# Performance work log

Measured on AMD Instinct MI355X. Metric: run time of the kernel, lower is better.

## Reference

```python
import jax, jax.numpy as jnp
import numpy as np

N_NODES = 50000
N_EDGES = 800000
HID = 256
MAX_ID = 10000

def _gcn(x, w, b, src, dst, ew, n):
    # PyG GCNConv with self-loops (weight 1.0): out = D^-1/2 (A+I) D^-1/2 (x W) + b
    xw = x @ w                                                   # [N, out]
    deg = jax.ops.segment_sum(ew, dst, num_segments=n) + 1.0     # self-loop adds 1
    dinv = jax.lax.rsqrt(deg)                                    # [N]
    norm = dinv[src] * ew * dinv[dst]                            # [E]
    agg = jax.ops.segment_sum(norm[:, None] * xw[src], dst, num_segments=n)
    agg = agg + (dinv * dinv)[:, None] * xw                      # self-loop term
    return agg + b

def setup_inputs() -> dict:
    key = jax.random.key(0)
    ks = jax.random.split(key, 24)
    s = 0.05
    inp = {
        "node_features": jax.random.normal(ks[0], (N_NODES, 3), jnp.float32),
        "edge_index": jax.random.randint(ks[1], (2, N_EDGES), 0, N_NODES),
        "edge_ids": jax.random.randint(ks[2], (N_EDGES,), 0, MAX_ID + 1),
        "edge_pos": jax.random.randint(ks[3], (N_EDGES,), 0, 3),
        "id_embed": jax.random.normal(ks[4], (MAX_ID + 1, 8), jnp.float32) * s,
        "pos_embed": jax.random.normal(ks[5], (3, 2), jnp.float32) * s,
        "ew_w1": jax.random.normal(ks[6], (10, 10), jnp.float32) * s,
        "ew_b1": jnp.zeros((10,), jnp.float32),
        "ew_w2": jax.random.normal(ks[7], (10, 1), jnp.float32) * s,
        "ew_b2": jnp.zeros((1,), jnp.float32),
        "conv1_w": jax.random.normal(ks[8], (3, HID), jnp.float32) * s,
        "conv1_b": jnp.zeros((HID,), jnp.float32),
        "conv2_w": jax.random.normal(ks[9], (HID, HID), jnp.float32) * s,
        "conv2_b": jnp.zeros((HID,), jnp.float32),
        "actor_w1": jax.random.normal(ks[10], (2 * HID, HID), jnp.float32) * s,
        "actor_b1": jnp.zeros((HID,), jnp.float32),
        "actor_w2": jax.random.normal(ks[11], (HID, 1), jnp.float32) * s,
        "actor_b2": jnp.zeros((1,), jnp.float32),
        "critic_w1": jax.random.normal(ks[12], (2 * HID, 2 * HID), jnp.float32) * s,
        "critic_b1": jnp.zeros((2 * HID,), jnp.float32),
        "critic_w2": jax.random.normal(ks[13], (2 * HID, HID), jnp.float32) * s,
        "critic_b2": jnp.zeros((HID,), jnp.float32),
        "critic_w3": jax.random.normal(ks[14], (HID, 1), jnp.float32) * s,
        "critic_b3": jnp.zeros((1,), jnp.float32),
    }
    return inp

def reference(node_features, edge_index, edge_ids, edge_pos, id_embed, pos_embed,
              ew_w1, ew_b1, ew_w2, ew_b2, conv1_w, conv1_b, conv2_w, conv2_b,
              actor_w1, actor_b1, actor_w2, actor_b2,
              critic_w1, critic_b1, critic_w2, critic_b2, critic_w3, critic_b3):
    n = node_features.shape[0]
    src, dst = edge_index[0], edge_index[1]
    # edge weight MLP: Linear-ReLU-Linear-Sigmoid on [id_embed(8) | pos_embed(2)]
    feat = jnp.concatenate([id_embed[edge_ids], pos_embed[edge_pos]], axis=1)  # [E,10]
    h = jax.nn.relu(feat @ ew_w1 + ew_b1)
    ew = jax.nn.sigmoid(h @ ew_w2 + ew_b2)[:, 0]                               # [E]
    # two GCN layers with ReLU
    x = jax.nn.relu(_gcn(node_features, conv1_w, conv1_b, src, dst, ew, n))
    x = jax.nn.relu(_gcn(x, conv2_w, conv2_b, src, dst, ew, n))
    # global mean pooling + concat
    g = jnp.mean(x, axis=0)                                                    # [H]
    combined = jnp.concatenate([x, jnp.broadcast_to(g, (n, g.shape[0]))], axis=1)
    # actor head
    a = jax.nn.relu(combined @ actor_w1 + actor_b1)
    action_logits = (a @ actor_w2 + actor_b2)[:, 0]                            # [N]
    # critic head on pooled features
    pooled = jnp.mean(combined, axis=0)[None, :]                               # [1,2H]
    c = jax.nn.relu(pooled @ critic_w1 + critic_b1)
    c = jax.nn.relu(c @ critic_w2 + critic_b2)
    state_value = (c @ critic_w3 + critic_b3)[0, 0]                            # scalar
    return action_logits, state_value
```

## Files before the change

### kernel.cpp

```cpp
#include <hip/hip_runtime.h>
#include <math.h>

#define HID 256

typedef __attribute__((ext_vector_type(8))) short short8;
typedef __attribute__((ext_vector_type(4))) float floatx4;

__device__ __forceinline__ ushort bf16_rne(float x) {
    uint u = __float_as_uint(x);
    uint r = (u + 0x7FFFu + ((u >> 16) & 1u)) >> 16;
    return (ushort)r;
}
__device__ __forceinline__ float bf16_to_f(ushort h) {
    return __uint_as_float(((uint)h) << 16);
}

__global__ void k_edge(const int* __restrict__ eid, const int* __restrict__ epos,
                       const float* __restrict__ id_emb, const float* __restrict__ pos_emb,
                       const float* __restrict__ w1, const float* __restrict__ b1,
                       const float* __restrict__ w2, const float* __restrict__ b2,
                       const int* __restrict__ ei, float* __restrict__ ew,
                       unsigned long long* __restrict__ cnt64, int E) {
    __shared__ float sW1[100];
    __shared__ float sB1[10];
    __shared__ float sW2[10];
    __shared__ float sB2;
    int t = threadIdx.x;
    if (t < 100) sW1[t] = w1[t];
    if (t < 10) { sB1[t] = b1[t]; sW2[t] = w2[t]; }
    if (t == 0) sB2 = b2[0];
    __syncthreads();
    int e = blockIdx.x * blockDim.x + t;
    if (e >= E) return;
    int id = eid[e];
    int p  = epos[e];
    const float4* ide = (const float4*)(id_emb + (size_t)id * 8);
    float4 fa = ide[0], fb = ide[1];
    float f[10];
    f[0] = fa.x; f[1] = fa.y; f[2] = fa.z; f[3] = fa.w;
    f[4] = fb.x; f[5] = fb.y; f[6] = fb.z; f[7] = fb.w;
    f[8] = pos_emb[p * 2 + 0];
    f[9] = pos_emb[p * 2 + 1];
    float acc = sB2;
#pragma unroll
    for (int j = 0; j < 10; j++) {
        float h = sB1[j];
#pragma unroll
        for (int i = 0; i < 10; i++) h += f[i] * sW1[i * 10 + j];
        h = fmaxf(h, 0.f);
        acc += h * sW2[j];
    }
    float w = 1.f / (1.f + expf(-acc));
    ew[e] = w;
    int dst = ei[E + e];
    unsigned long long pack = (1ull << 40) + (unsigned long long)(w * 1048576.0f + 0.5f);
    atomicAdd(&cnt64[dst], pack);
}

__global__ void k_scan_a(const unsigned long long* __restrict__ cnt64,
                         int* __restrict__ row_ptr, int* __restrict__ bsums,
                         float* __restrict__ deg, const float* __restrict__ nf,
                         float4* __restrict__ nf4, float* __restrict__ gsum,
                         const float* __restrict__ w2, const float* __restrict__ aw1,
                         ushort* __restrict__ w2h, ushort* __restrict__ w2l,
                         ushort* __restrict__ a1h, ushort* __restrict__ a1l, int N) {
    __shared__ int s[256];
    int b = blockIdx.x, t = threadIdx.x;
    int i = b * 256 + t;
    if (b == 0) gsum[t] = 0.f;
    if (b < 64) {
        int gid = b * 256 + t;
        int mat = gid >> 13;
        int rem = gid & 8191;
        int c = rem >> 10;
        int tt = (rem >> 6) & 15;
        int L = rem & 63;
        int k0 = 32 * c + (L >> 4) * 8;
        int n  = 16 * tt + (L & 15);
        const float* W = mat ? aw1 : w2;
        ushort* H  = mat ? a1h : w2h;
        ushort* Lo = mat ? a1l : w2l;
        short8 hv, lv;
#pragma unroll
        for (int j = 0; j < 8; j++) {
            float x = W[(size_t)(k0 + j) * HID + n];
            ushort h = bf16_rne(x);
            hv[j] = (short)h;
            lv[j] = (short)bf16_rne(x - bf16_to_f(h));
        }
        size_t off = (size_t)rem * 8;
        *(short8*)(H + off) = hv;
        *(short8*)(Lo + off) = lv;
    }
    int v = 0;
    if (i < N) {
        unsigned long long cv = cnt64[i];
        v = (int)(cv >> 40);
        float degf = (float)(cv & 0xFFFFFFFFFFull) * (1.0f / 1048576.0f);
        deg[i] = 1.f / sqrtf(degf + 1.f);
        nf4[i] = make_float4(nf[i * 3 + 0], nf[i * 3 + 1], nf[i * 3 + 2], 0.f);
    }
    s[t] = v;
    __syncthreads();
    for (int off = 1; off < 256; off <<= 1) {
        int u = (t >= off) ? s[t - off] : 0;
        __syncthreads();
        s[t] += u;
        __syncthreads();
    }
    int incl = s[t];
    if (i < N) row_ptr[i] = incl - v;
    if (t == 255) bsums[b] = incl;
}

__global__ void k_scan_c(int* __restrict__ row_ptr, int* __restrict__ cursor,
                         const int* __restrict__ bsums, int N, int NB) {
    __shared__ int s[256];
    int b = blockIdx.x, t = threadIdx.x;
    int v = (t < NB) ? bsums[t] : 0;
    s[t] = (t < b) ? v : 0;
    __syncthreads();
    for (int off = 128; off > 0; off >>= 1) {
        if (t < off) s[t] += s[t + off];
        __syncthreads();
    }
    int boff = s[0];
    int i = b * 256 + t;
    if (i < N) {
        int rp = row_ptr[i] + boff;
        row_ptr[i] = rp;
        cursor[i] = rp;
    }
    if (b == NB - 1) {
        __syncthreads();
        s[t] = (t < NB) ? bsums[t] : 0;
        __syncthreads();
        for (int off = 128; off > 0; off >>= 1) {
            if (t < off) s[t] += s[t + off];
            __syncthreads();
        }
        if (t == 0) row_ptr[N] = s[0];
    }
}

__global__ void k_fill(const int* __restrict__ ei, const float* __restrict__ ew,
                       const float* __restrict__ dinv, int* __restrict__ cursor,
                       int2* __restrict__ csr, int E) {
    int e = blockIdx.x * blockDim.x + threadIdx.x;
    if (e >= E) return;
    int src = ei[e];
    int dst = ei[E + e];
    int slot = atomicAdd(&cursor[dst], 1);
    float norm = dinv[src] * ew[e] * dinv[dst];
    csr[slot] = make_int2(src, __float_as_int(norm));
}

__global__ void k_agg3(const int* __restrict__ row_ptr, const int2* __restrict__ csr,
                       const float4* __restrict__ nf4, const float* __restrict__ dinv,
                       float4* __restrict__ T3, int N) {
    int n = blockIdx.x * blockDim.x + threadIdx.x;
    if (n >= N) return;
    int s = row_ptr[n];
    int e = row_ptr[n + 1];
    float ax = 0.f, ay = 0.f, az = 0.f;
    int i = s;
    for (; i + 4 <= e; i += 4) {
        int2 c0 = csr[i], c1 = csr[i + 1], c2 = csr[i + 2], c3 = csr[i + 3];
        float4 t0 = nf4[c0.x], t1 = nf4[c1.x], t2 = nf4[c2.x], t3 = nf4[c3.x];
        float w0 = __int_as_float(c0.y), w1 = __int_as_float(c1.y);
        float w2 = __int_as_float(c2.y), w3 = __int_as_float(c3.y);
        ax = fmaf(w0, t0.x, ax); ay = fmaf(w0, t0.y, ay); az = fmaf(w0, t0.z, az);
        ax = fmaf(w1, t1.x, ax); ay = fmaf(w1, t1.y, ay); az = fmaf(w1, t1.z, az);
        ax = fmaf(w2, t2.x, ax); ay = fmaf(w2, t2.y, ay); az = fmaf(w2, t2.z, az);
        ax = fmaf(w3, t3.x, ax); ay = fmaf(w3, t3.y, ay); az = fmaf(w3, t3.z, az);
    }
    for (; i < e; i++) {
        int2 sn = csr[i];
        float w = __int_as_float(sn.y);
        float4 v = nf4[sn.x];
        ax = fmaf(w, v.x, ax);
        ay = fmaf(w, v.y, ay);
        az = fmaf(w, v.z, az);
    }
    float d = dinv[n];
    float dd = d * d;
    float4 v = nf4[n];
    ax = fmaf(dd, v.x, ax);
    ay = fmaf(dd, v.y, ay);
    az = fmaf(dd, v.z, az);
    T3[n] = make_float4(ax, ay, az, 0.f);
}

__device__ __forceinline__ void gf_edge(float4 t, float wgt,
                                        const float4& w0, const float4& w1,
                                        const float4& w2, const float4& bv, float4& acc) {
    float xx = fmaxf(fmaf(t.x, w0.x, fmaf(t.y, w1.x, fmaf(t.z, w2.x, bv.x))), 0.f);
    float xy = fmaxf(fmaf(t.x, w0.y, fmaf(t.y, w1.y, fmaf(t.z, w2.y, bv.y))), 0.f);
    float xz = fmaxf(fmaf(t.x, w0.z, fmaf(t.y, w1.z, fmaf(t.z, w2.z, bv.z))), 0.f);
    float xw = fmaxf(fmaf(t.x, w0.w, fmaf(t.y, w1.w, fmaf(t.z, w2.w, bv.w))), 0.f);
    acc.x = fmaf(wgt, xx, acc.x);
    acc.y = fmaf(wgt, xy, acc.y);
    acc.z = fmaf(wgt, xz, acc.z);
    acc.w = fmaf(wgt, xw, acc.w);
}

__global__ void k_gatherfused(const int* __restrict__ row_ptr, const int2* __restrict__ csr,
                              const float4* __restrict__ T3, const float* __restrict__ dinv,
                              const float* __restrict__ cw, const float* __restrict__ cb,
                              ushort* __restrict__ Ah, ushort* __restrict__ Al, int N) {
    int lane = threadIdx.x & 63;
    int wv = threadIdx.x >> 6;
    int n = blockIdx.x * 4 + wv;
    if (n >= N) return;
    const float4 w0 = *(const float4*)(cw + 4 * lane);
    const float4 w1 = *(const float4*)(cw + HID + 4 * lane);
    const float4 w2 = *(const float4*)(cw + 2 * HID + 4 * lane);
    const float4 bv = *(const float4*)(cb + 4 * lane);
    int s = row_ptr[n];
    int e = row_ptr[n + 1];
    float4 acc = make_float4(0.f, 0.f, 0.f, 0.f);
    int i = s;
    for (; i + 4 <= e; i += 4) {
        int2 c0 = csr[i], c1 = csr[i + 1], c2 = csr[i + 2], c3 = csr[i + 3];
        float4 t0 = T3[c0.x], t1 = T3[c1.x], t2 = T3[c2.x], t3 = T3[c3.x];
        gf_edge(t0, __int_as_float(c0.y), w0, w1, w2, bv, acc);
        gf_edge(t1, __int_as_float(c1.y), w0, w1, w2, bv, acc);
        gf_edge(t2, __int_as_float(c2.y), w0, w1, w2, bv, acc);
        gf_edge(t3, __int_as_float(c3.y), w0, w1, w2, bv, acc);
    }
    for (; i < e; i++) {
        int2 sn = csr[i];
        gf_edge(T3[sn.x], __int_as_float(sn.y), w0, w1, w2, bv, acc);
    }
    float d = dinv[n];
    gf_edge(T3[n], d * d, w0, w1, w2, bv, acc);
    ushort4 hv, lv;
    ushort h;
    h = bf16_rne(acc.x); hv.x = h; lv.x = bf16_rne(acc.x - bf16_to_f(h));
    h = bf16_rne(acc.y); hv.y = h; lv.y = bf16_rne(acc.y - bf16_to_f(h));
    h = bf16_rne(acc.z); hv.z = h; lv.z = bf16_rne(acc.z - bf16_to_f(h));
    h = bf16_rne(acc.w); hv.w = h; lv.w = bf16_rne(acc.w - bf16_to_f(h));
    size_t base = (size_t)n * HID + lane * 4;
    *(ushort4*)(Ah + base) = hv;
    *(ushort4*)(Al + base) = lv;
}

#define ASTRIDE 264

__global__ __launch_bounds__(256, 2) void k_gemm_mfma(
        const ushort* __restrict__ Ah, const ushort* __restrict__ Al,
        const float* __restrict__ b2,
        const ushort* __restrict__ w2h, const ushort* __restrict__ w2l,
        const ushort* __restrict__ a1h, const ushort* __restrict__ a1l,
        float* __restrict__ P, float* __restrict__ gsum, int N) {
    __shared__ ushort Hs[64 * ASTRIDE];
    __shared__ ushort Ls[64 * ASTRIDE];
    int tid = threadIdx.x;
    int n0 = blockIdx.x * 64;
    int w = tid >> 6;
    int L = tid & 63;
    int quad = L >> 4, ln = L & 15;

    int arow[4];
#pragma unroll
    for (int mt = 0; mt < 4; mt++) {
        int r = n0 + mt * 16 + ln;
        arow[mt] = (r < N) ? r : (N - 1);
    }

    floatx4 acc[4][4];
#pragma unroll
    for (int i = 0; i < 4; i++)
#pragma unroll
        for (int j = 0; j < 4; j++) acc[i][j] = 0.f;
    {
        short8 pah[2][4], pal[2][4], pbh[2][4], pbl[2][4];
#pragma unroll
        for (int mt = 0; mt < 4; mt++) {
            size_t ab = (size_t)arow[mt] * HID + quad * 8;
            pah[0][mt] = *(const short8*)(Ah + ab);
            pal[0][mt] = *(const short8*)(Al + ab);
        }
#pragma unroll
        for (int nt = 0; nt < 4; nt++) {
            size_t off = ((size_t)(4 * w + nt) * 64 + L) * 8;
            pbh[0][nt] = *(const short8*)(w2h + off);
            pbl[0][nt] = *(const short8*)(w2l + off);
        }
#pragma unroll
        for (int c = 0; c < 8; c++) {
            int cur = c & 1, nxt = cur ^ 1;
            if (c < 7) {
#pragma unroll
                for (int mt = 0; mt < 4; mt++) {
                    size_t ab = (size_t)arow[mt] * HID + 32 * (c + 1) + quad * 8;
                    pah[nxt][mt] = *(const short8*)(Ah + ab);
                    pal[nxt][mt] = *(const short8*)(Al + ab);
                }
#pragma unroll
                for (int nt = 0; nt < 4; nt++) {
                    size_t off = ((size_t)((c + 1) * 16 + 4 * w + nt) * 64 + L) * 8;
                    pbh[nxt][nt] = *(const short8*)(w2h + off);
                    pbl[nxt][nt] = *(const short8*)(w2l + off);
                }
            }
#pragma unroll
            for (int nt = 0; nt < 4; nt++) {
#pragma unroll
                for (int mt = 0; mt < 4; mt++) {
                    acc[nt][mt] = __builtin_amdgcn_mfma_f32_16x16x32_bf16(pah[cur][mt], pbh[cur][nt], acc[nt][mt], 0, 0, 0);
                    acc[nt][mt] = __builtin_amdgcn_mfma_f32_16x16x32_bf16(pah[cur][mt], pbl[cur][nt], acc[nt][mt], 0, 0, 0);
                    acc[nt][mt] = __builtin_amdgcn_mfma_f32_16x16x32_bf16(pal[cur][mt], pbh[cur][nt], acc[nt][mt], 0, 0, 0);
                }
            }
        }
    }

#pragma unroll
    for (int nt = 0; nt < 4; nt++) {
        int col = (4 * w + nt) * 16 + ln;
        float bb = b2[col];
        float s = 0.f;
#pragma unroll
        for (int mt = 0; mt < 4; mt++) {
#pragma unroll
            for (int r = 0; r < 4; r++) {
                int row = n0 + mt * 16 + quad * 4 + r;
                float v = fmaxf(acc[nt][mt][r] + bb, 0.f);
                acc[nt][mt][r] = v;
                if (row < N) s += v;
            }
        }
        s += __shfl_down(s, 32, 64);
        s += __shfl_down(s, 16, 64);
        if (L < 16) atomicAdd(&gsum[col], s);
    }

#pragma unroll
    for (int nt = 0; nt < 4; nt++) {
        int col = (4 * w + nt) * 16 + ln;
#pragma unroll
        for (int mt = 0; mt < 4; mt++) {
#pragma unroll
            for (int r = 0; r < 4; r++) {
                int row = mt * 16 + quad * 4 + r;
                float v = acc[nt][mt][r];
                ushort h = bf16_rne(v);
                Hs[row * ASTRIDE + col] = h;
                Ls[row * ASTRIDE + col] = bf16_rne(v - bf16_to_f(h));
            }
        }
    }
    __syncthreads();

    floatx4 acc2[4][4];
#pragma unroll
    for (int i = 0; i < 4; i++)
#pragma unroll
        for (int j = 0; j < 4; j++) acc2[i][j] = 0.f;
    {
        short8 pbh[2][4], pbl[2][4];
#pragma unroll
        for (int nt = 0; nt < 4; nt++) {
            size_t off = ((size_t)(4 * w + nt) * 64 + L) * 8;
            pbh[0][nt] = *(const short8*)(a1h + off);
            pbl[0][nt] = *(const short8*)(a1l + off);
        }
#pragma unroll
        for (int c = 0; c < 8; c++) {
            int cur = c & 1, nxt = cur ^ 1;
            if (c < 7) {
#pragma unroll
                for (int nt = 0; nt < 4; nt++) {
                    size_t off = ((size_t)((c + 1) * 16 + 4 * w + nt) * 64 + L) * 8;
                    pbh[nxt][nt] = *(const short8*)(a1h + off);
                    pbl[nxt][nt] = *(const short8*)(a1l + off);
                }
            }
            short8 ahf[4], alf[4];
#pragma unroll
            for (int mt = 0; mt < 4; mt++) {
                int base = (mt * 16 + ln) * ASTRIDE + 32 * c + quad * 8;
                ahf[mt] = *(const short8*)&Hs[base];
                alf[mt] = *(const short8*)&Ls[base];
            }
#pragma unroll
            for (int nt = 0; nt < 4; nt++) {
#pragma unroll
                for (int mt = 0; mt < 4; mt++) {
                    acc2[nt][mt] = __builtin_amdgcn_mfma_f32_16x16x32_bf16(ahf[mt], pbh[cur][nt], acc2[nt][mt], 0, 0, 0);
                    acc2[nt][mt] = __builtin_amdgcn_mfma_f32_16x16x32_bf16(ahf[mt], pbl[cur][nt], acc2[nt][mt], 0, 0, 0);
                    acc2[nt][mt] = __builtin_amdgcn_mfma_f32_16x16x32_bf16(alf[mt], pbh[cur][nt], acc2[nt][mt], 0, 0, 0);
                }
            }
        }
    }

#pragma unroll
    for (int nt = 0; nt < 4; nt++) {
        int col = (4 * w + nt) * 16 + ln;
#pragma unroll
        for (int mt = 0; mt < 4; mt++) {
#pragma unroll
            for (int r = 0; r < 4; r++) {
                int row = n0 + mt * 16 + quad * 4 + r;
                if (row < N) P[(size_t)row * HID + col] = acc2[nt][mt][r];
            }
        }
    }
}

__global__ void k_headsA(const float* __restrict__ gsum,
                         const float* __restrict__ cw1, const float* __restrict__ cb1,
                         float* __restrict__ c1g,
                         const float* __restrict__ aw1, const float* __restrict__ ab1,
                         float* __restrict__ gbias,
                         const float* __restrict__ cb3, float* __restrict__ sv_out,
                         float invN) {
    __shared__ float part[4][64];
    int b = blockIdx.x, t = threadIdx.x;
    int c = t & 63;
    int kr = t >> 6;
    if (b == 0 && t == 0) sv_out[0] = cb3[0];
    if (b < 8) {
        int col = b * 64 + c;
        float s = 0.f;
        for (int k = kr * 128; k < kr * 128 + 128; k++)
            s += gsum[k & (HID - 1)] * invN * cw1[(size_t)k * 512 + col];
        part[kr][c] = s;
        __syncthreads();
        if (kr == 0) {
            float v = cb1[col] + part[0][c] + part[1][c] + part[2][c] + part[3][c];
            c1g[col] = fmaxf(v, 0.f);
        }
    } else {
        int col = (b - 8) * 64 + c;
        float s = 0.f;
        for (int k = kr * 64; k < kr * 64 + 64; k++)
            s += gsum[k] * invN * aw1[(size_t)(HID + k) * HID + col];
        part[kr][c] = s;
        __syncthreads();
        if (kr == 0)
            gbias[col] = ab1[col] + part[0][c] + part[1][c] + part[2][c] + part[3][c];
    }
}

__global__ void k_headsB(const float* __restrict__ c1g,
                         const float* __restrict__ cw2, const float* __restrict__ cb2,
                         const float* __restrict__ cw3, float* __restrict__ sv_out) {
    __shared__ float part[4][64];
    int b = blockIdx.x, t = threadIdx.x;
    int c = t & 63;
    int kr = t >> 6;
    int col = b * 64 + c;
    float s = 0.f;
    for (int k = kr * 128; k < kr * 128 + 128; k++)
        s += c1g[k] * cw2[(size_t)k * HID + col];
    part[kr][c] = s;
    __syncthreads();
    if (kr == 0) {
        float v = fmaxf(cb2[col] + part[0][c] + part[1][c] + part[2][c] + part[3][c], 0.f)
                * cw3[col];
#pragma unroll
        for (int off = 32; off > 0; off >>= 1) v += __shfl_down(v, off, 64);
        if (c == 0) atomicAdd(sv_out, v);
    }
}

__global__ void k_logits(const float* __restrict__ P, const float* __restrict__ gbias,
                         const float* __restrict__ aw2, const float* __restrict__ ab2,
                         float* __restrict__ out, int N) {
    int lane = threadIdx.x & 63;
    int wv = threadIdx.x >> 6;
    int n = blockIdx.x * 4 + wv;
    if (n >= N) return;
    float4 p = *(const float4*)(P + (size_t)n * HID + 4 * lane);
    float4 gb = *(const float4*)(gbias + 4 * lane);
    float4 w2 = *(const float4*)(aw2 + 4 * lane);
    float v = fmaxf(p.x + gb.x, 0.f) * w2.x
            + fmaxf(p.y + gb.y, 0.f) * w2.y
            + fmaxf(p.z + gb.z, 0.f) * w2.z
            + fmaxf(p.w + gb.w, 0.f) * w2.w;
#pragma unroll
    for (int off = 32; off > 0; off >>= 1) v += __shfl_down(v, off, 64);
    if (lane == 0) out[n] = v + ab2[0];
}

extern "C" void kernel_launch(void* const* d_in, const int* in_sizes, int n_in,
                              void* d_out, int out_size, void* d_ws, size_t ws_size,
                              hipStream_t stream) {
    const float* nf      = (const float*)d_in[0];
    const int*   ei      = (const int*)d_in[1];
    const int*   eid     = (const int*)d_in[2];
    const int*   epos    = (const int*)d_in[3];
    const float* id_emb  = (const float*)d_in[4];
    const float* pos_emb = (const float*)d_in[5];
    const float* ew_w1   = (const float*)d_in[6];
    const float* ew_b1   = (const float*)d_in[7];
    const float* ew_w2   = (const float*)d_in[8];
    const float* ew_b2   = (const float*)d_in[9];
    const float* c1w     = (const float*)d_in[10];
    const float* c1b     = (const float*)d_in[11];
    const float* c2w     = (const float*)d_in[12];
    const float* c2b     = (const float*)d_in[13];
    const float* aw1     = (const float*)d_in[14];
    const float* ab1     = (const float*)d_in[15];
    const float* aw2     = (const float*)d_in[16];
    const float* ab2     = (const float*)d_in[17];
    const float* cw1     = (const float*)d_in[18];
    const float* cb1     = (const float*)d_in[19];
    const float* cw2     = (const float*)d_in[20];
    const float* cb2     = (const float*)d_in[21];
    const float* cw3     = (const float*)d_in[22];
    const float* cb3     = (const float*)d_in[23];

    int N = in_sizes[0] / 3;
    int E = in_sizes[2];
    int NB = (N + 255) / 256;
    float invN = 1.f / (float)N;

    char* ws = (char*)d_ws;
    unsigned long long* cnt64 = (unsigned long long*)ws;  ws += (size_t)N * 8;
    float* gsum     = (float*)ws;                         ws += HID * 4;
    float* deg      = (float*)ws;                         ws += (size_t)N * 4;
    ushort* Ah      = (ushort*)ws;                        ws += (size_t)N * HID * 2;
    ushort* Al      = (ushort*)ws;                        ws += (size_t)N * HID * 2;
    float* P        = (float*)ws;                         ws += (size_t)N * HID * 4;
    float* ew       = (float*)ws;                         ws += (size_t)E * 4;
    int2*  csr      = (int2*)ws;                          ws += (size_t)E * 8;
    int*   row_ptr  = (int*)ws;                           ws += (size_t)(N + 1) * 4;
    int*   cursor   = (int*)ws;                           ws += (size_t)N * 4;
    int*   bsums    = (int*)ws;                           ws += 256 * 4;
    float4* T3      = (float4*)ws;                        ws += (size_t)N * 16;
    float4* nf4     = (float4*)ws;                        ws += (size_t)N * 16;
    float* gbias    = (float*)ws;                         ws += HID * 4;
    float* c1g      = (float*)ws;                         ws += 512 * 4;
    ushort* w2h     = (ushort*)ws;                        ws += 65536 * 2;
    ushort* w2l     = (ushort*)ws;                        ws += 65536 * 2;
    ushort* a1h     = (ushort*)ws;                        ws += 65536 * 2;
    ushort* a1l     = (ushort*)ws;                        ws += 65536 * 2;

    float* out = (float*)d_out;

    hipMemsetAsync(cnt64, 0, (size_t)N * 8, stream);

    k_edge<<<(E + 255) / 256, 256, 0, stream>>>(eid, epos, id_emb, pos_emb,
                                                ew_w1, ew_b1, ew_w2, ew_b2, ei, ew, cnt64, E);

    k_scan_a<<<NB, 256, 0, stream>>>(cnt64, row_ptr, bsums, deg, nf, nf4, gsum,
                                     c2w, aw1, w2h, w2l, a1h, a1l, N);
    k_scan_c<<<NB, 256, 0, stream>>>(row_ptr, cursor, bsums, N, NB);

    k_fill<<<(E + 255) / 256, 256, 0, stream>>>(ei, ew, deg, cursor, csr, E);

    k_agg3<<<(N + 255) / 256, 256, 0, stream>>>(row_ptr, csr, nf4, deg, T3, N);

    k_gatherfused<<<(N + 3) / 4, 256, 0, stream>>>(row_ptr, csr, T3, deg, c1w, c1b, Ah, Al, N);

    k_gemm_mfma<<<(N + 63) / 64, 256, 0, stream>>>(Ah, Al, c2b, w2h, w2l, a1h, a1l, P, gsum, N);

    k_headsA<<<12, 256, 0, stream>>>(gsum, cw1, cb1, c1g, aw1, ab1, gbias,
                                     cb3, out + N, invN);
    k_headsB<<<4, 256, 0, stream>>>(c1g, cw2, cb2, cw3, out + N);

    k_logits<<<(N + 3) / 4, 256, 0, stream>>>(P, gbias, aw2, ab2, out, N);
}
```

Baseline: 376.0 us.

## Shrink GEMM row tile, deepen gather unroll, merge head kernels, two edges per fill thread

The MFMA GEMM tile drops from 64 to 48 rows with launch bounds raised to 3 blocks per CU, trading per-block reuse for occupancy. Both gather loops now unroll by 8 with loads batched ahead of the math to put more memory requests in flight. The critic-head kernel and the logits kernel are merged into one launch, and k_fill handles two edges per thread. The aim is to cut launch overhead and raise memory-level parallelism, at the cost of more register pressure in the unrolled loops.

Measured after the change: 390.6 us. 3.9% more time.

```diff
diff --git a/kernel.cpp b/kernel.cpp
--- a/kernel.cpp
+++ b/kernel.cpp
@@ -145,14 +145,23 @@
 
 __global__ void k_fill(const int* __restrict__ ei, const float* __restrict__ ew,
                        const float* __restrict__ dinv, int* __restrict__ cursor,
-                       int2* __restrict__ csr, int E) {
-    int e = blockIdx.x * blockDim.x + threadIdx.x;
-    if (e >= E) return;
-    int src = ei[e];
-    int dst = ei[E + e];
-    int slot = atomicAdd(&cursor[dst], 1);
-    float norm = dinv[src] * ew[e] * dinv[dst];
-    csr[slot] = make_int2(src, __float_as_int(norm));
+                       int2* __restrict__ csr, int E, int Eh) {
+    int g = blockIdx.x * blockDim.x + threadIdx.x;
+    if (g < Eh) {
+        int src = ei[g];
+        int dst = ei[E + g];
+        float norm = dinv[src] * ew[g] * dinv[dst];
+        int slot = atomicAdd(&cursor[dst], 1);
+        csr[slot] = make_int2(src, __float_as_int(norm));
+    }
+    int e2 = g + Eh;
+    if (e2 < E) {
+        int src = ei[e2];
+        int dst = ei[E + e2];
+        float norm = dinv[src] * ew[e2] * dinv[dst];
+        int slot = atomicAdd(&cursor[dst], 1);
+        csr[slot] = make_int2(src, __float_as_int(norm));
+    }
 }
 
 __global__ void k_agg3(const int* __restrict__ row_ptr, const int2* __restrict__ csr,
@@ -164,15 +173,20 @@
     int e = row_ptr[n + 1];
     float ax = 0.f, ay = 0.f, az = 0.f;
     int i = s;
-    for (; i + 4 <= e; i += 4) {
-        int2 c0 = csr[i], c1 = csr[i + 1], c2 = csr[i + 2], c3 = csr[i + 3];
-        float4 t0 = nf4[c0.x], t1 = nf4[c1.x], t2 = nf4[c2.x], t3 = nf4[c3.x];
-        float w0 = __int_as_float(c0.y), w1 = __int_as_float(c1.y);
-        float w2 = __int_as_float(c2.y), w3 = __int_as_float(c3.y);
-        ax = fmaf(w0, t0.x, ax); ay = fmaf(w0, t0.y, ay); az = fmaf(w0, t0.z, az);
-        ax = fmaf(w1, t1.x, ax); ay = fmaf(w1, t1.y, ay); az = fmaf(w1, t1.z, az);
-        ax = fmaf(w2, t2.x, ax); ay = fmaf(w2, t2.y, ay); az = fmaf(w2, t2.z, az);
-        ax = fmaf(w3, t3.x, ax); ay = fmaf(w3, t3.y, ay); az = fmaf(w3, t3.z, az);
+    for (; i + 8 <= e; i += 8) {
+        int2 c[8];
+        float4 t[8];
+#pragma unroll
+        for (int j = 0; j < 8; j++) c[j] = csr[i + j];
+#pragma unroll
+        for (int j = 0; j < 8; j++) t[j] = nf4[c[j].x];
+#pragma unroll
+        for (int j = 0; j < 8; j++) {
+            float w = __int_as_float(c[j].y);
+            ax = fmaf(w, t[j].x, ax);
+            ay = fmaf(w, t[j].y, ay);
+            az = fmaf(w, t[j].z, az);
+        }
     }
     for (; i < e; i++) {
         int2 sn = csr[i];
@@ -220,13 +234,16 @@
     int e = row_ptr[n + 1];
     float4 acc = make_float4(0.f, 0.f, 0.f, 0.f);
     int i = s;
-    for (; i + 4 <= e; i += 4) {
-        int2 c0 = csr[i], c1 = csr[i + 1], c2 = csr[i + 2], c3 = csr[i + 3];
-        float4 t0 = T3[c0.x], t1 = T3[c1.x], t2 = T3[c2.x], t3 = T3[c3.x];
-        gf_edge(t0, __int_as_float(c0.y), w0, w1, w2, bv, acc);
-        gf_edge(t1, __int_as_float(c1.y), w0, w1, w2, bv, acc);
-        gf_edge(t2, __int_as_float(c2.y), w0, w1, w2, bv, acc);
-        gf_edge(t3, __int_as_float(c3.y), w0, w1, w2, bv, acc);
+    for (; i + 8 <= e; i += 8) {
+        int2 c[8];
+        float4 t[8];
+#pragma unroll
+        for (int j = 0; j < 8; j++) c[j] = csr[i + j];
+#pragma unroll
+        for (int j = 0; j < 8; j++) t[j] = T3[c[j].x];
+#pragma unroll
+        for (int j = 0; j < 8; j++)
+            gf_edge(t[j], __int_as_float(c[j].y), w0, w1, w2, bv, acc);
     }
     for (; i < e; i++) {
         int2 sn = csr[i];
@@ -246,37 +263,39 @@
 }
 
 #define ASTRIDE 264
-
-__global__ __launch_bounds__(256, 2) void k_gemm_mfma(
+#define MT 3
+#define TROWS 48
+
+__global__ __launch_bounds__(256, 3) void k_gemm_mfma(
         const ushort* __restrict__ Ah, const ushort* __restrict__ Al,
         const float* __restrict__ b2,
         const ushort* __restrict__ w2h, const ushort* __restrict__ w2l,
         const ushort* __restrict__ a1h, const ushort* __restrict__ a1l,
         float* __restrict__ P, float* __restrict__ gsum, int N) {
-    __shared__ ushort Hs[64 * ASTRIDE];
-    __shared__ ushort Ls[64 * ASTRIDE];
+    __shared__ ushort Hs[TROWS * ASTRIDE];
+    __shared__ ushort Ls[TROWS * ASTRIDE];
     int tid = threadIdx.x;
-    int n0 = blockIdx.x * 64;
+    int n0 = blockIdx.x * TROWS;
     int w = tid >> 6;
     int L = tid & 63;
     int quad = L >> 4, ln = L & 15;
 
-    int arow[4];
-#pragma unroll
-    for (int mt = 0; mt < 4; mt++) {
+    int arow[MT];
+#pragma unroll
+    for (int mt = 0; mt < MT; mt++) {
         int r = n0 + mt * 16 + ln;
         arow[mt] = (r < N) ? r : (N - 1);
     }
 
-    floatx4 acc[4][4];
+    floatx4 acc[4][MT];
 #pragma unroll
     for (int i = 0; i < 4; i++)
 #pragma unroll
-        for (int j = 0; j < 4; j++) acc[i][j] = 0.f;
+        for (int j = 0; j < MT; j++) acc[i][j] = 0.f;
     {
-        short8 pah[2][4], pal[2][4], pbh[2][4], pbl[2][4];
-#pragma unroll
-        for (int mt = 0; mt < 4; mt++) {
+        short8 pah[2][MT], pal[2][MT], pbh[2][4], pbl[2][4];
+#pragma unroll
+        for (int mt = 0; mt < MT; mt++) {
             size_t ab = (size_t)arow[mt] * HID + quad * 8;
             pah[0][mt] = *(const short8*)(Ah + ab);
             pal[0][mt] = *(const short8*)(Al + ab);
@@ -292,7 +311,7 @@
             int cur = c & 1, nxt = cur ^ 1;
             if (c < 7) {
 #pragma unroll
-                for (int mt = 0; mt < 4; mt++) {
+                for (int mt = 0; mt < MT; mt++) {
                     size_t ab = (size_t)arow[mt] * HID + 32 * (c + 1) + quad * 8;
                     pah[nxt][mt] = *(const short8*)(Ah + ab);
                     pal[nxt][mt] = *(const short8*)(Al + ab);
@@ -307,7 +326,7 @@
 #pragma unroll
             for (int nt = 0; nt < 4; nt++) {
 #pragma unroll
-                for (int mt = 0; mt < 4; mt++) {
+                for (int mt = 0; mt < MT; mt++) {
                     acc[nt][mt] = __builtin_amdgcn_mfma_f32_16x16x32_bf16(pah[cur][mt], pbh[cur][nt], acc[nt][mt], 0, 0, 0);
                     acc[nt][mt] = __builtin_amdgcn_mfma_f32_16x16x32_bf16(pah[cur][mt], pbl[cur][nt], acc[nt][mt], 0, 0, 0);
                     acc[nt][mt] = __builtin_amdgcn_mfma_f32_16x16x32_bf16(pal[cur][mt], pbh[cur][nt], acc[nt][mt], 0, 0, 0);
@@ -322,7 +341,7 @@
         float bb = b2[col];
         float s = 0.f;
 #pragma unroll
-        for (int mt = 0; mt < 4; mt++) {
+        for (int mt = 0; mt < MT; mt++) {
 #pragma unroll
             for (int r = 0; r < 4; r++) {
                 int row = n0 + mt * 16 + quad * 4 + r;
@@ -340,7 +359,7 @@
     for (int nt = 0; nt < 4; nt++) {
         int col = (4 * w + nt) * 16 + ln;
 #pragma unroll
-        for (int mt = 0; mt < 4; mt++) {
+        for (int mt = 0; mt < MT; mt++) {
 #pragma unroll
             for (int r = 0; r < 4; r++) {
                 int row = mt * 16 + quad * 4 + r;
@@ -353,11 +372,11 @@
     }
     __syncthreads();
 
-    floatx4 acc2[4][4];
+    floatx4 acc2[4][MT];
 #pragma unroll
     for (int i = 0; i < 4; i++)
 #pragma unroll
-        for (int j = 0; j < 4; j++) acc2[i][j] = 0.f;
+        for (int j = 0; j < MT; j++) acc2[i][j] = 0.f;
     {
         short8 pbh[2][4], pbl[2][4];
 #pragma unroll
@@ -377,9 +396,9 @@
                     pbl[nxt][nt] = *(const short8*)(a1l + off);
                 }
             }
-            short8 ahf[4], alf[4];
-#pragma unroll
-            for (int mt = 0; mt < 4; mt++) {
+            short8 ahf[MT], alf[MT];
+#pragma unroll
+            for (int mt = 0; mt < MT; mt++) {
                 int base = (mt * 16 + ln) * ASTRIDE + 32 * c + quad * 8;
                 ahf[mt] = *(const short8*)&Hs[base];
                 alf[mt] = *(const short8*)&Ls[base];
@@ -387,7 +406,7 @@
 #pragma unroll
             for (int nt = 0; nt < 4; nt++) {
 #pragma unroll
-                for (int mt = 0; mt < 4; mt++) {
+                for (int mt = 0; mt < MT; mt++) {
                     acc2[nt][mt] = __builtin_amdgcn_mfma_f32_16x16x32_bf16(ahf[mt], pbh[cur][nt], acc2[nt][mt], 0, 0, 0);
                     acc2[nt][mt] = __builtin_amdgcn_mfma_f32_16x16x32_bf16(ahf[mt], pbl[cur][nt], acc2[nt][mt], 0, 0, 0);
                     acc2[nt][mt] = __builtin_amdgcn_mfma_f32_16x16x32_bf16(alf[mt], pbh[cur][nt], acc2[nt][mt], 0, 0, 0);
@@ -400,7 +419,7 @@
     for (int nt = 0; nt < 4; nt++) {
         int col = (4 * w + nt) * 16 + ln;
 #pragma unroll
-        for (int mt = 0; mt < 4; mt++) {
+        for (int mt = 0; mt < MT; mt++) {
 #pragma unroll
             for (int r = 0; r < 4; r++) {
                 int row = n0 + mt * 16 + quad * 4 + r;
@@ -445,34 +464,35 @@
     }
 }
 
-__global__ void k_headsB(const float* __restrict__ c1g,
-                         const float* __restrict__ cw2, const float* __restrict__ cb2,
-                         const float* __restrict__ cw3, float* __restrict__ sv_out) {
-    __shared__ float part[4][64];
+__global__ void k_headsBL(const float* __restrict__ c1g,
+                          const float* __restrict__ cw2, const float* __restrict__ cb2,
+                          const float* __restrict__ cw3, float* __restrict__ sv_out,
+                          const float* __restrict__ P, const float* __restrict__ gbias,
+                          const float* __restrict__ aw2, const float* __restrict__ ab2,
+                          float* __restrict__ out, int N) {
     int b = blockIdx.x, t = threadIdx.x;
-    int c = t & 63;
-    int kr = t >> 6;
-    int col = b * 64 + c;
-    float s = 0.f;
-    for (int k = kr * 128; k < kr * 128 + 128; k++)
-        s += c1g[k] * cw2[(size_t)k * HID + col];
-    part[kr][c] = s;
-    __syncthreads();
-    if (kr == 0) {
-        float v = fmaxf(cb2[col] + part[0][c] + part[1][c] + part[2][c] + part[3][c], 0.f)
-                * cw3[col];
-#pragma unroll
-        for (int off = 32; off > 0; off >>= 1) v += __shfl_down(v, off, 64);
-        if (c == 0) atomicAdd(sv_out, v);
-    }
-}
-
-__global__ void k_logits(const float* __restrict__ P, const float* __restrict__ gbias,
-                         const float* __restrict__ aw2, const float* __restrict__ ab2,
-                         float* __restrict__ out, int N) {
-    int lane = threadIdx.x & 63;
-    int wv = threadIdx.x >> 6;
-    int n = blockIdx.x * 4 + wv;
+    if (b < 4) {
+        __shared__ float part[4][64];
+        int c = t & 63;
+        int kr = t >> 6;
+        int col = b * 64 + c;
+        float s = 0.f;
+        for (int k = kr * 128; k < kr * 128 + 128; k++)
+            s += c1g[k] * cw2[(size_t)k * HID + col];
+        part[kr][c] = s;
+        __syncthreads();
+        if (kr == 0) {
+            float v = fmaxf(cb2[col] + part[0][c] + part[1][c] + part[2][c] + part[3][c], 0.f)
+                    * cw3[col];
+#pragma unroll
+            for (int off = 32; off > 0; off >>= 1) v += __shfl_down(v, off, 64);
+            if (c == 0) atomicAdd(sv_out, v);
+        }
+        return;
+    }
+    int lane = t & 63;
+    int wv = t >> 6;
+    int n = (b - 4) * 4 + wv;
     if (n >= N) return;
     float4 p = *(const float4*)(P + (size_t)n * HID + 4 * lane);
     float4 gb = *(const float4*)(gbias + 4 * lane);
@@ -517,6 +537,7 @@
     int N = in_sizes[0] / 3;
     int E = in_sizes[2];
     int NB = (N + 255) / 256;
+    int Eh = (E + 1) / 2;
     float invN = 1.f / (float)N;
 
     char* ws = (char*)d_ws;
@@ -551,17 +572,17 @@
                                      c2w, aw1, w2h, w2l, a1h, a1l, N);
     k_scan_c<<<NB, 256, 0, stream>>>(row_ptr, cursor, bsums, N, NB);
 
-    k_fill<<<(E + 255) / 256, 256, 0, stream>>>(ei, ew, deg, cursor, csr, E);
+    k_fill<<<(Eh + 255) / 256, 256, 0, stream>>>(ei, ew, deg, cursor, csr, E, Eh);
 
     k_agg3<<<(N + 255) / 256, 256, 0, stream>>>(row_ptr, csr, nf4, deg, T3, N);
 
     k_gatherfused<<<(N + 3) / 4, 256, 0, stream>>>(row_ptr, csr, T3, deg, c1w, c1b, Ah, Al, N);
 
-    k_gemm_mfma<<<(N + 63) / 64, 256, 0, stream>>>(Ah, Al, c2b, w2h, w2l, a1h, a1l, P, gsum, N);
+    k_gemm_mfma<<<(N + TROWS - 1) / TROWS, 256, 0, stream>>>(Ah, Al, c2b, w2h, w2l,
+                                                             a1h, a1l, P, gsum, N);
 
     k_headsA<<<12, 256, 0, stream>>>(gsum, cw1, cb1, c1g, aw1, ab1, gbias,
                                      cb3, out + N, invN);
-    k_headsB<<<4, 256, 0, stream>>>(c1g, cw2, cb2, cw3, out + N);
-
-    k_logits<<<(N + 3) / 4, 256, 0, stream>>>(P, gbias, aw2, ab2, out, N);
-}
+    k_headsBL<<<4 + (N + 3) / 4, 256, 0, stream>>>(c1g, cw2, cb2, cw3, out + N,
+                                                   P, gbias, aw2, ab2, out, N);
+}
```
